# Performance work log

Measured on AMD Instinct MI355X. Metric: run time of the kernel, lower is better.

## Reference

```python
import jax, jax.numpy as jnp
import numpy as np

TAU = 0.07
EPS = 1e-10


def setup_inputs() -> dict:
    key = jax.random.key(0)
    k1, k2 = jax.random.split(key)
    N, D = 8192, 128
    features = jax.random.normal(k1, (N, D), dtype=jnp.float32)
    alpha = jnp.float32(0.5)  # cosine-similarity threshold in (-1, 1)
    return {"features": features, "alpha": alpha}


def reference(features, alpha):
    # L2-normalize rows (torch F.normalize uses eps=1e-12 clamp on the norm)
    norm = jnp.maximum(jnp.linalg.norm(features, axis=1, keepdims=True), 1e-12)
    f = features / norm
    sim = f @ f.T  # [N, N]

    n = f.shape[0]
    not_eye = ~jnp.eye(n, dtype=bool)
    pos_mask = (sim >= alpha) & not_eye
    neg_mask = (sim < alpha) & not_eye

    e = jnp.exp(sim / TAU)  # [N, N], computed once and reused for both masks
    numerator = jnp.sum(jnp.where(pos_mask, e, 0.0), axis=1) + EPS
    denominator = numerator + jnp.sum(jnp.where(neg_mask, e, 0.0), axis=1) + EPS
    loss = -jnp.log(numerator / denominator)
    return loss.mean()
```

## Files before the change

kernel.cpp:

```cpp
#include <hip/hip_runtime.h>

#define N_ROWS 8192
#define BM 128
#define SEG 512
#define TILE 64
#define NTILE (SEG / TILE)
#define NSEG (N_ROWS / SEG)
#define NPART NSEG
#define KEXP 20.60992915f

typedef __attribute__((ext_vector_type(4))) float f32x4;
typedef __attribute__((ext_vector_type(2))) long long2v;

__device__ __forceinline__ float fast_exp2(float x) {
  float r;
  asm("v_exp_f32 %0, %1" : "=v"(r) : "v"(x));
  return r;
}

__global__ __launch_bounds__(256) void knorm(const float* __restrict__ feat,
                                             unsigned short* __restrict__ fnA,
                                             unsigned short* __restrict__ fnB) {
  const int wid = threadIdx.x >> 6;
  const int lane = threadIdx.x & 63;
  const int row = blockIdx.x * 4 + wid;
  const float2 v = *(const float2*)(feat + (size_t)row * 128 + lane * 2);
  float s = v.x * v.x + v.y * v.y;
#pragma unroll
  for (int m = 1; m < 64; m <<= 1) s += __shfl_xor(s, m);
  const float inv = 1.0f / fmaxf(sqrtf(s), 1e-12f);
  const float x = v.x * inv, y = v.y * inv;
  const int k = lane * 2;
  const int p = k >> 6, h = (k >> 5) & 1, ksub = (k >> 3) & 3, kk = k & 7;
  const int byteoff = ((row >> 4) << 11) + (p << 10) + (ksub << 8) +
                      ((row & 15) << 4) + (h << 3) + kk;
  const unsigned int pkB = __builtin_amdgcn_cvt_pk_fp8_f32(x, y, 0, 0);
  const unsigned int pkA = __builtin_amdgcn_cvt_pk_fp8_f32(x * KEXP, y * KEXP, 0, 0);
  fnB[byteoff >> 1] = (unsigned short)pkB;
  fnA[byteoff >> 1] = (unsigned short)pkA;
}

__global__ __launch_bounds__(256, 4) void ksim(const unsigned short* __restrict__ fnA,
                                               const unsigned short* __restrict__ fnB,
                                               const float* __restrict__ alphap,
                                               float* __restrict__ posP,
                                               float* __restrict__ totP) {
  const int tid = threadIdx.x;
  const int lane = tid & 63;
  const int wid = tid >> 6;
  const int r0 = blockIdx.x * BM;
  const int c0 = blockIdx.y * SEG;
  const float alphaK = alphap[0] * KEXP;

  const char* __restrict__ FA = (const char*)fnA;
  const char* __restrict__ FB = (const char*)fnB;

  long aR[2][4];
  {
    const int G0 = (r0 + wid * 32) >> 4;
#pragma unroll
    for (int m = 0; m < 2; m++)
#pragma unroll
      for (int p = 0; p < 2; p++) {
        const long2v t = *(const long2v*)(FA + (size_t)(G0 + m) * 2048 + p * 1024 + lane * 16);
        aR[m][2 * p] = t[0];
        aR[m][2 * p + 1] = t[1];
      }
  }

  float pp[2][4] = {{0.f}}, tp[2][4] = {{0.f}};

#pragma unroll 1
  for (int it = 0; it < NTILE; ++it) {
    const char* Bb = FB + (size_t)((c0 >> 4) + it * 4) * 2048 + lane * 16;

    f32x4 acc[2][4];
#pragma unroll
    for (int m = 0; m < 2; m++)
#pragma unroll
      for (int n = 0; n < 4; n++) acc[m][n] = (f32x4){0.f, 0.f, 0.f, 0.f};

#pragma unroll
    for (int p = 0; p < 2; p++) {
      const long2v b0 = *(const long2v*)(Bb + 0 * 2048 + p * 1024);
      const long2v b1 = *(const long2v*)(Bb + 1 * 2048 + p * 1024);
      const long2v b2 = *(const long2v*)(Bb + 2 * 2048 + p * 1024);
      const long2v b3 = *(const long2v*)(Bb + 3 * 2048 + p * 1024);
#pragma unroll
      for (int m = 0; m < 2; m++) {
        acc[m][0] = __builtin_amdgcn_mfma_f32_16x16x32_fp8_fp8(aR[m][2 * p], b0[0], acc[m][0], 0, 0, 0);
        acc[m][1] = __builtin_amdgcn_mfma_f32_16x16x32_fp8_fp8(aR[m][2 * p], b1[0], acc[m][1], 0, 0, 0);
        acc[m][2] = __builtin_amdgcn_mfma_f32_16x16x32_fp8_fp8(aR[m][2 * p], b2[0], acc[m][2], 0, 0, 0);
        acc[m][3] = __builtin_amdgcn_mfma_f32_16x16x32_fp8_fp8(aR[m][2 * p], b3[0], acc[m][3], 0, 0, 0);
        acc[m][0] = __builtin_amdgcn_mfma_f32_16x16x32_fp8_fp8(aR[m][2 * p + 1], b0[1], acc[m][0], 0, 0, 0);
        acc[m][1] = __builtin_amdgcn_mfma_f32_16x16x32_fp8_fp8(aR[m][2 * p + 1], b1[1], acc[m][1], 0, 0, 0);
        acc[m][2] = __builtin_amdgcn_mfma_f32_16x16x32_fp8_fp8(aR[m][2 * p + 1], b2[1], acc[m][2], 0, 0, 0);
        acc[m][3] = __builtin_amdgcn_mfma_f32_16x16x32_fp8_fp8(aR[m][2 * p + 1], b3[1], acc[m][3], 0, 0, 0);
      }
    }

    const int cb = c0 + it * TILE;
#pragma unroll
    for (int m = 0; m < 2; m++) {
      const int grb = r0 + wid * 32 + m * 16;
#pragma unroll
      for (int n = 0; n < 4; n++) {
        const int gcb = cb + n * 16;
        const f32x4 a = acc[m][n];
        if (grb == gcb) {
          const int gr0 = (lane >> 4) << 2;
          const int gcl = lane & 15;
#pragma unroll
          for (int r = 0; r < 4; r++) {
            const float e = fast_exp2(a[r]);
            const float ev = (gr0 + r == gcl) ? 0.0f : e;
            tp[m][r] += ev;
            pp[m][r] += (a[r] >= alphaK) ? ev : 0.0f;
          }
        } else {
#pragma unroll
          for (int r = 0; r < 4; r++) {
            const float e = fast_exp2(a[r]);
            tp[m][r] += e;
            pp[m][r] += (a[r] >= alphaK) ? e : 0.0f;
          }
        }
      }
    }
  }

#pragma unroll
  for (int m = 0; m < 2; m++)
#pragma unroll
    for (int r = 0; r < 4; r++) {
      float p = pp[m][r], t = tp[m][r];
#pragma unroll
      for (int msk = 1; msk < 16; msk <<= 1) {
        p += __shfl_xor(p, msk);
        t += __shfl_xor(t, msk);
      }
      if ((lane & 15) == 0) {
        const int row = r0 + wid * 32 + m * 16 + ((lane >> 4) << 2) + r;
        posP[blockIdx.y * N_ROWS + row] = p;
        totP[blockIdx.y * N_ROWS + row] = t;
      }
    }
}

__global__ __launch_bounds__(128) void kred1(const float* __restrict__ posP,
                                             const float* __restrict__ totP,
                                             float* __restrict__ bp) {
  const int t = threadIdx.x;
  const int row = blockIdx.x * 128 + t;
  float pos = 0.f, tot = 0.f;
#pragma unroll
  for (int c = 0; c < NPART; c++) {
    pos += posP[c * N_ROWS + row];
    tot += totP[c * N_ROWS + row];
  }
  float term = __logf(tot + 2e-10f) - __logf(pos + 1e-10f);
#pragma unroll
  for (int m = 1; m < 64; m <<= 1) term += __shfl_xor(term, m);
  __shared__ float s2[2];
  if ((t & 63) == 0) s2[t >> 6] = term;
  __syncthreads();
  if (t == 0) bp[blockIdx.x] = s2[0] + s2[1];
}

__global__ void kred2(const float* __restrict__ bp, float* __restrict__ out) {
  const int l = threadIdx.x;
  float v = bp[l];
#pragma unroll
  for (int m = 1; m < 64; m <<= 1) v += __shfl_xor(v, m);
  if (l == 0) out[0] = v * (1.0f / 8192.0f);
}

extern "C" void kernel_launch(void* const* d_in, const int* in_sizes, int n_in,
                              void* d_out, int out_size, void* d_ws, size_t ws_size,
                              hipStream_t stream) {
  const float* feat = (const float*)d_in[0];
  const float* alphap = (const float*)d_in[1];
  char* ws = (char*)d_ws;
  unsigned short* fnA = (unsigned short*)ws;
  unsigned short* fnB = (unsigned short*)(ws + (1u << 20));
  float* posP = (float*)(ws + (2u << 20));
  float* totP = (float*)(ws + (3u << 20));
  float* bp = (float*)(ws + (4u << 20));
  float* out = (float*)d_out;

  knorm<<<dim3(N_ROWS / 4), dim3(256), 0, stream>>>(feat, fnA, fnB);
  ksim<<<dim3(N_ROWS / BM, NSEG), dim3(256), 0, stream>>>(fnA, fnB, alphap, posP, totP);
  kred1<<<dim3(N_ROWS / 128), dim3(128), 0, stream>>>(posP, totP, bp);
  kred2<<<dim3(1), dim3(64), 0, stream>>>(bp, out);
}
```

Before: 35.14 us.

## Fuse final reductions via last-block atomic counter and swap ksim grid axes

Merges the two reduction kernels into one: each block publishes its partial with a release store, bumps an atomic counter, and the last block sums all partials and writes the mean. This removes one kernel launch but adds a hipMemsetAsync to reset the counter. The ksim grid is also transposed so consecutive blocks share the same row block and walk different column segments, which changes which blocks run together and how they hit L2.

```diff
diff --git a/kernel.cpp b/kernel.cpp
--- a/kernel.cpp
+++ b/kernel.cpp
@@ -48,8 +48,8 @@
   const int tid = threadIdx.x;
   const int lane = tid & 63;
   const int wid = tid >> 6;
-  const int r0 = blockIdx.x * BM;
-  const int c0 = blockIdx.y * SEG;
+  const int r0 = blockIdx.y * BM;
+  const int c0 = blockIdx.x * SEG;
   const float alphaK = alphap[0] * KEXP;
 
   const char* __restrict__ FA = (const char*)fnA;
@@ -141,15 +141,17 @@
       }
       if ((lane & 15) == 0) {
         const int row = r0 + wid * 32 + m * 16 + ((lane >> 4) << 2) + r;
-        posP[blockIdx.y * N_ROWS + row] = p;
-        totP[blockIdx.y * N_ROWS + row] = t;
-      }
-    }
-}
-
-__global__ __launch_bounds__(128) void kred1(const float* __restrict__ posP,
-                                             const float* __restrict__ totP,
-                                             float* __restrict__ bp) {
+        posP[blockIdx.x * N_ROWS + row] = p;
+        totP[blockIdx.x * N_ROWS + row] = t;
+      }
+    }
+}
+
+__global__ __launch_bounds__(128) void kred(const float* __restrict__ posP,
+                                            const float* __restrict__ totP,
+                                            float* __restrict__ bp,
+                                            unsigned int* __restrict__ counter,
+                                            float* __restrict__ out) {
   const int t = threadIdx.x;
   const int row = blockIdx.x * 128 + t;
   float pos = 0.f, tot = 0.f;
@@ -162,17 +164,25 @@
 #pragma unroll
   for (int m = 1; m < 64; m <<= 1) term += __shfl_xor(term, m);
   __shared__ float s2[2];
+  __shared__ unsigned int sOld;
   if ((t & 63) == 0) s2[t >> 6] = term;
   __syncthreads();
-  if (t == 0) bp[blockIdx.x] = s2[0] + s2[1];
-}
-
-__global__ void kred2(const float* __restrict__ bp, float* __restrict__ out) {
-  const int l = threadIdx.x;
-  float v = bp[l];
-#pragma unroll
-  for (int m = 1; m < 64; m <<= 1) v += __shfl_xor(v, m);
-  if (l == 0) out[0] = v * (1.0f / 8192.0f);
+  if (t == 0) {
+    __hip_atomic_store(&bp[blockIdx.x], s2[0] + s2[1], __ATOMIC_RELEASE,
+                       __HIP_MEMORY_SCOPE_AGENT);
+    sOld = __hip_atomic_fetch_add(counter, 1u, __ATOMIC_ACQ_REL,
+                                  __HIP_MEMORY_SCOPE_AGENT);
+  }
+  __syncthreads();
+  if (sOld == 63 && t < 64) {
+    float v = __hip_atomic_load(&bp[t], __ATOMIC_ACQUIRE, __HIP_MEMORY_SCOPE_AGENT);
+#pragma unroll
+    for (int m = 1; m < 64; m <<= 1) v += __shfl_xor(v, m);
+    if (t == 0) {
+      out[0] = v * (1.0f / 8192.0f);
+      __hip_atomic_store(counter, 0u, __ATOMIC_RELEASE, __HIP_MEMORY_SCOPE_AGENT);
+    }
+  }
 }
 
 extern "C" void kernel_launch(void* const* d_in, const int* in_sizes, int n_in,
@@ -186,10 +196,11 @@
   float* posP = (float*)(ws + (2u << 20));
   float* totP = (float*)(ws + (3u << 20));
   float* bp = (float*)(ws + (4u << 20));
+  unsigned int* counter = (unsigned int*)(ws + (4u << 20) + 4096);
   float* out = (float*)d_out;
 
+  hipMemsetAsync(counter, 0, sizeof(unsigned int), stream);
   knorm<<<dim3(N_ROWS / 4), dim3(256), 0, stream>>>(feat, fnA, fnB);
-  ksim<<<dim3(N_ROWS / BM, NSEG), dim3(256), 0, stream>>>(fnA, fnB, alphap, posP, totP);
-  kred1<<<dim3(N_ROWS / 128), dim3(128), 0, stream>>>(posP, totP, bp);
-  kred2<<<dim3(1), dim3(64), 0, stream>>>(bp, out);
-}
+  ksim<<<dim3(NSEG, N_ROWS / BM), dim3(256), 0, stream>>>(fnA, fnB, alphap, posP, totP);
+  kred<<<dim3(N_ROWS / 128), dim3(128), 0, stream>>>(posP, totP, bp, counter, out);
+}
```

Result: slower. 39.14 us (+11.4%).

## Exploit similarity-matrix symmetry by computing only upper-triangular block panels

Applied to the files above, without the earlier changes.

The similarity kernel now runs on a square grid of 128x128 block panels. Blocks below the diagonal exit immediately, and each off-diagonal block writes both its row partial sums and its column partial sums, reduced through shared memory. This roughly halves the MFMA and exp work across the N×N matrix. In exchange, the partial-sum buffers grow four times larger, the reduction kernel reads more data, and half the launched blocks do nothing. Column sums reuse the asymmetric pair (A scaled by the exponent constant, B unscaled), which adds a small extra fp8 rounding difference.

```diff
diff --git a/kernel.cpp b/kernel.cpp
--- a/kernel.cpp
+++ b/kernel.cpp
@@ -2,11 +2,8 @@
 
 #define N_ROWS 8192
 #define BM 128
-#define SEG 512
-#define TILE 64
-#define NTILE (SEG / TILE)
-#define NSEG (N_ROWS / SEG)
-#define NPART NSEG
+#define NPANEL (N_ROWS / BM)
+#define NPART NPANEL
 #define KEXP 20.60992915f
 
 typedef __attribute__((ext_vector_type(4))) float f32x4;
@@ -45,11 +42,15 @@
                                                const float* __restrict__ alphap,
                                                float* __restrict__ posP,
                                                float* __restrict__ totP) {
+  const int I = blockIdx.x;
+  const int J = blockIdx.y;
+  if (J < I) return;
+  __shared__ float colbuf[4][2][128];
   const int tid = threadIdx.x;
   const int lane = tid & 63;
   const int wid = tid >> 6;
-  const int r0 = blockIdx.x * BM;
-  const int c0 = blockIdx.y * SEG;
+  const int r0 = I * BM;
+  const int c0 = J * BM;
   const float alphaK = alphap[0] * KEXP;
 
   const char* __restrict__ FA = (const char*)fnA;
@@ -71,7 +72,7 @@
   float pp[2][4] = {{0.f}}, tp[2][4] = {{0.f}};
 
 #pragma unroll 1
-  for (int it = 0; it < NTILE; ++it) {
+  for (int it = 0; it < 2; ++it) {
     const char* Bb = FB + (size_t)((c0 >> 4) + it * 4) * 2048 + lane * 16;
 
     f32x4 acc[2][4];
@@ -99,7 +100,8 @@
       }
     }
 
-    const int cb = c0 + it * TILE;
+    float cpp[4] = {0.f, 0.f, 0.f, 0.f}, ctp[4] = {0.f, 0.f, 0.f, 0.f};
+    const int cb = c0 + it * 64;
 #pragma unroll
     for (int m = 0; m < 2; m++) {
       const int grb = r0 + wid * 32 + m * 16;
@@ -114,17 +116,36 @@
           for (int r = 0; r < 4; r++) {
             const float e = fast_exp2(a[r]);
             const float ev = (gr0 + r == gcl) ? 0.0f : e;
+            const float pev = (a[r] >= alphaK) ? ev : 0.0f;
             tp[m][r] += ev;
-            pp[m][r] += (a[r] >= alphaK) ? ev : 0.0f;
+            pp[m][r] += pev;
+            ctp[n] += ev;
+            cpp[n] += pev;
           }
         } else {
 #pragma unroll
           for (int r = 0; r < 4; r++) {
             const float e = fast_exp2(a[r]);
+            const float pev = (a[r] >= alphaK) ? e : 0.0f;
             tp[m][r] += e;
-            pp[m][r] += (a[r] >= alphaK) ? e : 0.0f;
+            pp[m][r] += pev;
+            ctp[n] += e;
+            cpp[n] += pev;
           }
         }
+      }
+    }
+
+#pragma unroll
+    for (int n = 0; n < 4; n++) {
+      float cp = cpp[n], ct = ctp[n];
+      cp += __shfl_xor(cp, 16);
+      cp += __shfl_xor(cp, 32);
+      ct += __shfl_xor(ct, 16);
+      ct += __shfl_xor(ct, 32);
+      if (lane < 16) {
+        colbuf[wid][0][it * 64 + n * 16 + lane] = cp;
+        colbuf[wid][1][it * 64 + n * 16 + lane] = ct;
       }
     }
   }
@@ -141,10 +162,21 @@
       }
       if ((lane & 15) == 0) {
         const int row = r0 + wid * 32 + m * 16 + ((lane >> 4) << 2) + r;
-        posP[blockIdx.y * N_ROWS + row] = p;
-        totP[blockIdx.y * N_ROWS + row] = t;
-      }
-    }
+        posP[(size_t)J * N_ROWS + row] = p;
+        totP[(size_t)J * N_ROWS + row] = t;
+      }
+    }
+
+  __syncthreads();
+  if (I != J && tid < 128) {
+    const int colg = c0 + tid;
+    const float cp = colbuf[0][0][tid] + colbuf[1][0][tid] +
+                     colbuf[2][0][tid] + colbuf[3][0][tid];
+    const float ct = colbuf[0][1][tid] + colbuf[1][1][tid] +
+                     colbuf[2][1][tid] + colbuf[3][1][tid];
+    posP[(size_t)I * N_ROWS + colg] = cp;
+    totP[(size_t)I * N_ROWS + colg] = ct;
+  }
 }
 
 __global__ __launch_bounds__(128) void kred1(const float* __restrict__ posP,
@@ -155,8 +187,8 @@
   float pos = 0.f, tot = 0.f;
 #pragma unroll
   for (int c = 0; c < NPART; c++) {
-    pos += posP[c * N_ROWS + row];
-    tot += totP[c * N_ROWS + row];
+    pos += posP[(size_t)c * N_ROWS + row];
+    tot += totP[(size_t)c * N_ROWS + row];
   }
   float term = __logf(tot + 2e-10f) - __logf(pos + 1e-10f);
 #pragma unroll
@@ -184,12 +216,12 @@
   unsigned short* fnA = (unsigned short*)ws;
   unsigned short* fnB = (unsigned short*)(ws + (1u << 20));
   float* posP = (float*)(ws + (2u << 20));
-  float* totP = (float*)(ws + (3u << 20));
-  float* bp = (float*)(ws + (4u << 20));
+  float* totP = (float*)(ws + (4u << 20));
+  float* bp = (float*)(ws + (6u << 20));
   float* out = (float*)d_out;
 
   knorm<<<dim3(N_ROWS / 4), dim3(256), 0, stream>>>(feat, fnA, fnB);
-  ksim<<<dim3(N_ROWS / BM, NSEG), dim3(256), 0, stream>>>(fnA, fnB, alphap, posP, totP);
+  ksim<<<dim3(NPANEL, NPANEL), dim3(256), 0, stream>>>(fnA, fnB, alphap, posP, totP);
   kred1<<<dim3(N_ROWS / 128), dim3(128), 0, stream>>>(posP, totP, bp);
   kred2<<<dim3(1), dim3(64), 0, stream>>>(bp, out);
 }
```

Measured after the change: 62.98 us. 79.2% more time.
